# Kernel optimization log

Hardware: AMD Instinct MI355X
Metric: run time of the kernel (lower is better)

Reference implementation:

```python
import jax, jax.numpy as jnp
import numpy as np
from jax import lax

FC = 8      # heads_count
LN_EPS = 1e-5

def _ln(x, g, b):
    mu = jnp.mean(x, axis=-1, keepdims=True)
    var = jnp.mean((x - mu) ** 2, axis=-1, keepdims=True)
    return (x - mu) / jnp.sqrt(var + LN_EPS) * g + b

def _l2norm(x):
    return x / jnp.maximum(jnp.linalg.norm(x, axis=-1, keepdims=True), 1e-12)

def _gelu(x):
    return jax.nn.gelu(x, approximate=False)

def _resize_bilinear(x, oh, ow):
    # x: [N, C, H, W], align_corners=True bilinear (matches F.interpolate)
    h, w = x.shape[2], x.shape[3]
    ys = jnp.linspace(0.0, h - 1.0, oh)
    xs = jnp.linspace(0.0, w - 1.0, ow)
    y0 = jnp.floor(ys).astype(jnp.int32); y1 = jnp.minimum(y0 + 1, h - 1)
    x0 = jnp.floor(xs).astype(jnp.int32); x1 = jnp.minimum(x0 + 1, w - 1)
    dy = (ys - y0).astype(x.dtype)[None, None, :, None]
    dx = (xs - x0).astype(x.dtype)[None, None, None, :]
    rows = x[:, :, y0, :] * (1 - dy) + x[:, :, y1, :] * dy
    return rows[:, :, :, x0] * (1 - dx) + rows[:, :, :, x1] * dx

def _merge_block(x, center, h, w, p):
    # x: [n,l,c], center: [n,s,c]
    n, l, c = x.shape
    hc, wc = h // 2, w // 2
    xn = x.transpose(0, 2, 1).reshape(n, c, h, w)
    cn = center.transpose(0, 2, 1).reshape(n, c, hc, wc)
    up = _resize_bilinear(cn, h, w)
    y = jnp.concatenate([xn, up], axis=1)            # [n,2c,h,w]
    y = y.transpose(0, 2, 3, 1)                      # NHWC
    y = _gelu(y @ p['mb_l0_w'] + p['mb_l0_b'])
    y = y @ p['mb_l1_w'] + p['mb_l1_b']              # [n,h,w,c]
    y = y.transpose(0, 3, 1, 2)                      # NCHW
    mu = jnp.mean(y, axis=(1, 2, 3), keepdims=True)  # GroupNorm(1, c)
    var = jnp.mean((y - mu) ** 2, axis=(1, 2, 3), keepdims=True)
    y = (y - mu) / jnp.sqrt(var + LN_EPS) * p['mb_gn_g'][None, :, None, None] + p['mb_gn_b'][None, :, None, None]
    down = _resize_bilinear(y, hc, wc)
    new_x = y.reshape(n, c, h * w).transpose(0, 2, 1) + x
    new_c = down.reshape(n, c, hc * wc).transpose(0, 2, 1) + center
    return new_x, new_c

def _global_cluster(x0, center1, p):
    n, l, c = x0.shape
    s = center1.shape[1]
    xp = x0 @ p['gc_p0_w'] + p['gc_p0_b']            # [n,l,hd]
    cp = center1 @ p['gc_p1_w'] + p['gc_p1_b']       # [n,s,2hd]
    hd = xp.shape[-1]
    sc = hd // FC
    m = n * FC
    xp = xp.reshape(n, l, FC, sc).transpose(0, 2, 1, 3).reshape(m, l, sc)
    cp = cp.reshape(n, s, FC, 2 * sc).transpose(0, 2, 1, 3).reshape(m, s, 2 * sc)
    cpt, cval = cp[..., :sc], cp[..., sc:]
    sim = jnp.einsum('mlc,msc->mls', _l2norm(xp), _l2norm(cpt))
    sim = jax.nn.sigmoid(p['gc_alpha'] * sim + p['gc_beta'])
    vals = jnp.max(sim, axis=2)                      # [m,l]
    idx = jnp.argmax(sim, axis=2)                    # [m,l]
    disp = vals[..., None] * jnp.take_along_axis(cval, idx[:, :, None], axis=1)  # [m,l,sc]
    disp = disp.reshape(n, FC, l, sc).transpose(0, 2, 1, 3).reshape(n, l, FC * sc)
    return disp @ p['gc_m_w'] + p['gc_m_b']

def _global_block(x0, center1, h, w, p):
    n, l, c = x0.shape
    new = _global_cluster(x0, center1, p)
    new = _ln(new, p['gb_n0_g'], p['gb_n0_b'])
    y = jnp.concatenate([x0, new], axis=2)           # [n,l,2c]
    y = y.reshape(n, h, w, 2 * c)
    y = _gelu(y @ p['gb_lin_w'] + p['gb_lin_b'])     # [n,h,w,2c]
    y = y.transpose(0, 3, 1, 2)                      # NCHW
    y = lax.conv_general_dilated(y, p['gb_conv_w'], (1, 1), ((1, 1), (1, 1)),
                                 dimension_numbers=('NCHW', 'OIHW', 'NCHW'))
    y = y + p['gb_conv_b'][None, :, None, None]
    y = y.reshape(n, c, h * w).transpose(0, 2, 1)    # [n,l,c]
    return _ln(y, p['gb_n1_g'], p['gb_n1_b']) + x0

def setup_inputs() -> dict:
    key = jax.random.key(0)
    ks = jax.random.split(key, 24)
    N, H, W, C, HD = 8, 52, 52, 256, 256
    L = H * W
    S = (H // 2) * (W // 2)
    f32 = jnp.float32
    def xav(k, shape, fin, fout):
        a = (6.0 / (fin + fout)) ** 0.5
        return jax.random.uniform(k, shape, minval=-a, maxval=a, dtype=f32)
    return {
        'x0_16x': jax.random.normal(ks[0], (N, L, C), f32),
        'x1_16x': jax.random.normal(ks[1], (N, L, C), f32),
        'x0_32x': jax.random.normal(ks[2], (N, S, C), f32),
        'x1_32x': jax.random.normal(ks[3], (N, S, C), f32),
        'size0_16x': 52, 'size1_16x': 52,
        'mb_l0_w': xav(ks[4], (2 * C, 2 * C), 2 * C, 2 * C), 'mb_l0_b': jnp.zeros((2 * C,), f32),
        'mb_l1_w': xav(ks[5], (2 * C, C), 2 * C, C), 'mb_l1_b': jnp.zeros((C,), f32),
        'mb_gn_g': jnp.ones((C,), f32), 'mb_gn_b': jnp.zeros((C,), f32),
        'gc_p0_w': xav(ks[6], (C, HD), C, HD), 'gc_p0_b': jnp.zeros((HD,), f32),
        'gc_p1_w': xav(ks[7], (C, 2 * HD), C, 2 * HD), 'gc_p1_b': jnp.zeros((2 * HD,), f32),
        'gc_m_w': xav(ks[8], (HD, C), HD, C), 'gc_m_b': jnp.zeros((C,), f32),
        'gc_alpha': jnp.ones((1,), f32), 'gc_beta': jnp.zeros((1,), f32),
        'gb_n0_g': jnp.ones((C,), f32), 'gb_n0_b': jnp.zeros((C,), f32),
        'gb_lin_w': xav(ks[9], (2 * C, 2 * C), 2 * C, 2 * C), 'gb_lin_b': jnp.zeros((2 * C,), f32),
        'gb_conv_w': xav(ks[10], (C, 2 * C, 3, 3), 2 * C * 9, C * 9), 'gb_conv_b': jnp.zeros((C,), f32),
        'gb_n1_g': jnp.ones((C,), f32), 'gb_n1_b': jnp.zeros((C,), f32),
    }

def reference(x0_16x, x1_16x, x0_32x, x1_32x, size0_16x, size1_16x,
              mb_l0_w, mb_l0_b, mb_l1_w, mb_l1_b, mb_gn_g, mb_gn_b,
              gc_p0_w, gc_p0_b, gc_p1_w, gc_p1_b, gc_m_w, gc_m_b, gc_alpha, gc_beta,
              gb_n0_g, gb_n0_b, gb_lin_w, gb_lin_b, gb_conv_w, gb_conv_b, gb_n1_g, gb_n1_b):
    p = dict(mb_l0_w=mb_l0_w, mb_l0_b=mb_l0_b, mb_l1_w=mb_l1_w, mb_l1_b=mb_l1_b,
             mb_gn_g=mb_gn_g, mb_gn_b=mb_gn_b,
             gc_p0_w=gc_p0_w, gc_p0_b=gc_p0_b, gc_p1_w=gc_p1_w, gc_p1_b=gc_p1_b,
             gc_m_w=gc_m_w, gc_m_b=gc_m_b, gc_alpha=gc_alpha, gc_beta=gc_beta,
             gb_n0_g=gb_n0_g, gb_n0_b=gb_n0_b, gb_lin_w=gb_lin_w, gb_lin_b=gb_lin_b,
             gb_conv_w=gb_conv_w, gb_conv_b=gb_conv_b, gb_n1_g=gb_n1_g, gb_n1_b=gb_n1_b)
    h0 = w0 = int(size0_16x)
    h1 = w1 = int(size1_16x)
    # single layer, type == 'cross' (types=["cross"]); shared weights across streams
    x0_16x, x0_32x = _merge_block(x0_16x, x0_32x, h0, w0, p)
    x1_16x, x1_32x = _merge_block(x1_16x, x1_32x, h1, w1, p)
    x0_16x = _global_block(x0_16x, x1_32x, h0, w0, p)
    x1_16x = _global_block(x1_16x, x0_32x, h1, w1, p)
    return (x0_16x, x1_16x)
```

## Files before the change

kernel.cpp:

```cpp
#include <hip/hip_runtime.h>
#include <math.h>

#define NB 8
#define HH 52
#define WW 52
#define LL 2704
#define CC 256
#define HC 26
#define WC 26
#define SS 676
#define C2 512
#define FCn 8
#define SCn 32
#define M16 (NB*LL)
#define M32 (NB*SS)
#define KCONV (9*C2)
#define SAMP16 ((size_t)LL*CC)
#define SAMP32 ((size_t)SS*CC)

typedef double dvec4 __attribute__((ext_vector_type(4)));
typedef float  f32x4 __attribute__((ext_vector_type(4)));
typedef short  b16x8 __attribute__((ext_vector_type(8)));

__device__ __forceinline__ float  gelu_ct(float x){ return 0.5f*x*(1.0f + erff(x*0.70710678118654752f)); }
__device__ __forceinline__ double gelu_ct(double x){ return 0.5*x*(1.0 + erf(x*0.70710678118654752440)); }

__device__ __forceinline__ short f2b(float x){
    union { float f; unsigned u; } v; v.f = x;
    unsigned r = v.u + 0x7fffu + ((v.u >> 16) & 1u);
    return (short)(r >> 16);
}

template<typename TA0, typename TO, bool GELU, bool ADDB, bool UPS>
__global__ __launch_bounds__(256) void gemm_d64(
    const TA0* __restrict__ A0,
    const float* __restrict__ W, const float* __restrict__ Bias,
    const double* __restrict__ cw,
    TO* __restrict__ Out, int M, int K, int N)
{
    __shared__ double As[16][130];
    __shared__ double Bs[16][66];
    const int t = threadIdx.x;
    const int mBase = blockIdx.y * 128;
    const int nBase = blockIdx.x * 64;
    const int arow = t >> 1;
    const int kofA = (t & 1) << 3;
    const int kb   = t >> 4;
    const int nof  = (t & 15) << 2;
    const int w  = t >> 6;
    const int lane = t & 63;
    const int lr = lane & 15, lk = lane >> 4;

    dvec4 prm = {0.,0.,0.,0.}, prn = {0.,0.,0.,0.};
    prm = __builtin_amdgcn_mfma_f64_16x16x4f64((double)lr, 0.25, prm, 0,0,0);
    prn = __builtin_amdgcn_mfma_f64_16x16x4f64(0.25, (double)lr, prn, 0,0,0);
    int pm[4], pn[4];
    #pragma unroll
    for (int i=0;i<4;i++){ pm[i] = (int)prm[i]; pn[i] = (int)prn[i]; }

    dvec4 acc[2][4];
    #pragma unroll
    for (int rf=0;rf<2;rf++)
        #pragma unroll
        for (int cb=0;cb<4;cb++) acc[rf][cb] = (dvec4){0.,0.,0.,0.};

    const int am = mBase + arow;
    double aReg[8], bReg[4];
    auto loadA = [&](int k0){
        #pragma unroll
        for (int j=0;j<8;j++){
            int k = k0 + kofA + j;
            aReg[j] = (am < M) ? (double)A0[(size_t)am*K + k] : 0.0;
        }
    };
    auto loadB = [&](int k0){
        #pragma unroll
        for (int j=0;j<4;j++)
            bReg[j] = (double)W[(size_t)(k0+kb)*N + nBase + nof + j];
    };
    loadA(0); loadB(0);
    for (int k0 = 0; k0 < K; k0 += 16){
        __syncthreads();
        #pragma unroll
        for (int j=0;j<8;j++) As[kofA+j][arow] = aReg[j];
        #pragma unroll
        for (int j=0;j<4;j++) Bs[kb][nof+j] = bReg[j];
        __syncthreads();
        if (k0 + 16 < K){ loadA(k0+16); loadB(k0+16); }
        #pragma unroll
        for (int ks = 0; ks < 4; ks++){
            double a0 = As[ks*4+lk][w*32 + lr];
            double a1 = As[ks*4+lk][w*32 + 16 + lr];
            double b0 = Bs[ks*4+lk][lr];
            double b1 = Bs[ks*4+lk][16 + lr];
            double b2 = Bs[ks*4+lk][32 + lr];
            double b3 = Bs[ks*4+lk][48 + lr];
            acc[0][0] = __builtin_amdgcn_mfma_f64_16x16x4f64(a0,b0,acc[0][0],0,0,0);
            acc[0][1] = __builtin_amdgcn_mfma_f64_16x16x4f64(a0,b1,acc[0][1],0,0,0);
            acc[0][2] = __builtin_amdgcn_mfma_f64_16x16x4f64(a0,b2,acc[0][2],0,0,0);
            acc[0][3] = __builtin_amdgcn_mfma_f64_16x16x4f64(a0,b3,acc[0][3],0,0,0);
            acc[1][0] = __builtin_amdgcn_mfma_f64_16x16x4f64(a1,b0,acc[1][0],0,0,0);
            acc[1][1] = __builtin_amdgcn_mfma_f64_16x16x4f64(a1,b1,acc[1][1],0,0,0);
            acc[1][2] = __builtin_amdgcn_mfma_f64_16x16x4f64(a1,b2,acc[1][2],0,0,0);
            acc[1][3] = __builtin_amdgcn_mfma_f64_16x16x4f64(a1,b3,acc[1][3],0,0,0);
        }
    }
    #pragma unroll
    for (int rf=0;rf<2;rf++){
        #pragma unroll
        for (int i=0;i<4;i++){
            const int row = mBase + w*32 + rf*16 + pm[i];
            if (row >= M) continue;
            int nloc = 0, y0=0, y1=0, x0=0, x1=0;
            double dy=0.0, dx=0.0;
            if (UPS){
                nloc = row / LL;
                int l = row - nloc*LL;
                int hh = l / WW, ww2 = l - hh*WW;
                double fy = (hh==HH-1) ? (double)(HC-1) : hh*((double)(HC-1)/(HH-1));
                double fx = (ww2==WW-1) ? (double)(WC-1) : ww2*((double)(WC-1)/(WW-1));
                y0 = (int)fy; y1 = min(y0+1, HC-1);
                x0 = (int)fx; x1 = min(x0+1, WC-1);
                dy = fy - y0; dx = fx - x0;
            }
            #pragma unroll
            for (int cb=0;cb<4;cb++){
                const int col = nBase + cb*16 + pn[i];
                double v = acc[rf][cb][i];
                if (UPS){
                    const double* cb0 = cw + ((size_t)nloc*SS)*N + col;
                    double v00 = cb0[(size_t)(y0*WC + x0)*N];
                    double v01 = cb0[(size_t)(y0*WC + x1)*N];
                    double v10 = cb0[(size_t)(y1*WC + x0)*N];
                    double v11 = cb0[(size_t)(y1*WC + x1)*N];
                    double r0 = v00*(1.0-dy) + v10*dy;
                    double r1 = v01*(1.0-dy) + v11*dy;
                    v += r0*(1.0-dx) + r1*dx;
                }
                if (ADDB) v += (double)Bias[col];
                if (GELU) v = gelu_ct(v);
                Out[(size_t)row*N + col] = (TO)v;
            }
        }
    }
}

template<bool GELU, bool CAT, bool OUT_BF>
__global__ __launch_bounds__(256) void gemm_bf(
    const short* __restrict__ A0, const short* __restrict__ A1, int K0,
    const short* __restrict__ Wb, const float* __restrict__ Bias,
    void* __restrict__ OutV, int M, int K, int N)
{
    __shared__ short As[64][72];
    __shared__ short Bs[64][72];
    const int t = threadIdx.x;
    const int mBase = blockIdx.y*64, nBase = blockIdx.x*64;
    const int lane = t & 63, lr = lane & 15, lg = lane >> 4;
    const int wr = (t >> 6) * 16;
    const int srow = t >> 2;
    const int sk   = (t & 3) * 16;
    const int am = mBase + srow;
    const int bo = nBase + srow;
    f32x4 acc[4] = {{0,0,0,0},{0,0,0,0},{0,0,0,0},{0,0,0,0}};

    for (int c0 = 0; c0 < K; c0 += 64){
        const int kk = c0 + sk;
        const short* ap;
        if (!CAT || kk < K0) ap = A0 + (size_t)am*K0 + kk;
        else                 ap = A1 + (size_t)am*(K-K0) + (kk - K0);
        b16x8 a0 = *(const b16x8*)ap;
        b16x8 a1 = *(const b16x8*)(ap + 8);
        b16x8 bv0 = *(const b16x8*)&Wb[(size_t)bo*K + kk];
        b16x8 bv1 = *(const b16x8*)&Wb[(size_t)bo*K + kk + 8];
        __syncthreads();
        *(b16x8*)&As[srow][sk]     = a0;
        *(b16x8*)&As[srow][sk + 8] = a1;
        *(b16x8*)&Bs[srow][sk]     = bv0;
        *(b16x8*)&Bs[srow][sk + 8] = bv1;
        __syncthreads();
        #pragma unroll
        for (int kc=0;kc<2;kc++){
            b16x8 a = *(const b16x8*)&As[wr + lr][kc*32 + lg*8];
            #pragma unroll
            for (int cb=0;cb<4;cb++){
                b16x8 b = *(const b16x8*)&Bs[cb*16 + lr][kc*32 + lg*8];
                acc[cb] = __builtin_amdgcn_mfma_f32_16x16x32_bf16(a, b, acc[cb], 0,0,0);
            }
        }
    }
    #pragma unroll
    for (int cb=0;cb<4;cb++){
        int col = nBase + cb*16 + lr;
        float bias = Bias[col];
        #pragma unroll
        for (int i=0;i<4;i++){
            int row = mBase + wr + lg*4 + i;
            float v = acc[cb][i] + bias;
            if (GELU) v = gelu_ct(v);
            if (OUT_BF) ((short*)OutV)[(size_t)row*N + col] = f2b(v);
            else        ((float*)OutV)[(size_t)row*N + col] = v;
        }
    }
}

__global__ __launch_bounds__(256) void conv_bf2(const short* __restrict__ Xb,
    const short* __restrict__ WTb, const float* __restrict__ Bias, float* __restrict__ Out)
{
    __shared__ short As[32][72];
    __shared__ short Bs[256][72];
    const int t = threadIdx.x;
    const int mBase = blockIdx.x*32;
    const int lane = t & 63, lr = lane & 15, lg = lane >> 4;
    const int w = t >> 6;
    const int wr16 = (w & 1) * 16;
    const int ch   = (w >> 1) * 8;
    const int arow = t >> 3;
    const int ska  = (t & 7) * 8;
    const int srow = t >> 2;
    const int sk   = (t & 3) * 16;
    const int am = mBase + arow;
    const int an = am / LL; const int ahw = am % LL;
    const int ah = ahw / WW; const int aw = ahw % WW;
    f32x4 acc[8];
    #pragma unroll
    for (int i=0;i<8;i++) acc[i] = (f32x4){0.f,0.f,0.f,0.f};
    const b16x8 z = {0,0,0,0,0,0,0,0};

    for (int pos = 0; pos < 9; pos++){
        const int dh = pos/3 - 1, dw = pos%3 - 1;
        const int h2 = ah + dh, w2 = aw + dw;
        const bool ok = (h2 >= 0 && h2 < HH && w2 >= 0 && w2 < WW);
        const short* xrow = Xb + ((size_t)(an*LL + h2*WW + w2))*C2;
        for (int c0 = 0; c0 < C2; c0 += 64){
            b16x8 a0 = ok ? *(const b16x8*)&xrow[c0 + ska] : z;
            b16x8 w0[4], w1[4];
            #pragma unroll
            for (int r=0;r<4;r++){
                const short* wp = WTb + (size_t)(srow + 64*r)*KCONV + pos*C2 + c0 + sk;
                w0[r] = *(const b16x8*)wp;
                w1[r] = *(const b16x8*)(wp + 8);
            }
            __syncthreads();
            *(b16x8*)&As[arow][ska] = a0;
            #pragma unroll
            for (int r=0;r<4;r++){
                *(b16x8*)&Bs[srow + 64*r][sk]     = w0[r];
                *(b16x8*)&Bs[srow + 64*r][sk + 8] = w1[r];
            }
            __syncthreads();
            #pragma unroll
            for (int kc=0;kc<2;kc++){
                b16x8 a = *(const b16x8*)&As[wr16 + lr][kc*32 + lg*8];
                #pragma unroll
                for (int cb=0;cb<8;cb++){
                    b16x8 b = *(const b16x8*)&Bs[(ch+cb)*16 + lr][kc*32 + lg*8];
                    acc[cb] = __builtin_amdgcn_mfma_f32_16x16x32_bf16(a, b, acc[cb], 0,0,0);
                }
            }
        }
    }
    #pragma unroll
    for (int cb=0;cb<8;cb++){
        int col = (ch+cb)*16 + lr;
        float bias = Bias[col];
        #pragma unroll
        for (int i=0;i<4;i++){
            int row = mBase + wr16 + lg*4 + i;
            Out[(size_t)row*CC + col] = acc[cb][i] + bias;
        }
    }
}

__global__ void wtransb_k(const float* __restrict__ wsrc, short* __restrict__ wt){
    int o = blockIdx.x;
    int i = threadIdx.x;
    #pragma unroll
    for (int pos = 0; pos < 9; pos++)
        wt[(size_t)o*KCONV + pos*C2 + i] = f2b(wsrc[((size_t)o*C2 + i)*9 + pos]);
}

__global__ void wtb_k(const float* __restrict__ src, short* __restrict__ dst, int K, int N){
    int n = blockIdx.x;
    for (int k = threadIdx.x; k < K; k += 256)
        dst[(size_t)n*K + k] = f2b(src[(size_t)k*N + n]);
}

__global__ void d2b_k(const double* __restrict__ src, short* __restrict__ dst){
    int i = blockIdx.x*256 + threadIdx.x;
    dst[i] = f2b((float)src[i]);
}

__global__ __launch_bounds__(256) void gn_stats_k(const double* __restrict__ t2c,
    double* __restrict__ stats, int nOff){
    const double* p = t2c + (size_t)blockIdx.y*SAMP16;
    int i0 = blockIdx.x*4096 + threadIdx.x;
    double s = 0.0, q = 0.0;
    #pragma unroll
    for (int r = 0; r < 16; r++){
        double v = p[i0 + r*256];
        s += v; q += v*v;
    }
    #pragma unroll
    for (int off = 32; off; off >>= 1){
        s += __shfl_xor(s, off);
        q += __shfl_xor(q, off);
    }
    __shared__ double ls[4], lq[4];
    int wid = threadIdx.x >> 6;
    if ((threadIdx.x & 63) == 0){ ls[wid] = s; lq[wid] = q; }
    __syncthreads();
    if (threadIdx.x == 0){
        int n = nOff + blockIdx.y;
        atomicAdd(&stats[n*2+0], ls[0]+ls[1]+ls[2]+ls[3]);
        atomicAdd(&stats[n*2+1], lq[0]+lq[1]+lq[2]+lq[3]);
    }
}

__global__ void merge_x_k(const double* __restrict__ t2c, const float* __restrict__ x,
    const float* __restrict__ g, const float* __restrict__ b,
    const double* __restrict__ stats, int nOff, double* __restrict__ mxn){
    int idx = blockIdx.x*256 + threadIdx.x;
    const double inv = 1.0/((double)LL*CC);
    int c = idx & (CC-1);
    int n = nOff + idx / (LL*CC);
    double mu = stats[2*n]*inv;
    double var = stats[2*n+1]*inv - mu*mu;
    double r = 1.0/sqrt(var + 1e-5);
    mxn[idx] = (t2c[idx]-mu)*r*(double)g[c] + (double)b[c] + (double)x[idx];
}

__global__ void merge_c_k(const double* __restrict__ t2c, const float* __restrict__ cen,
    const float* __restrict__ g, const float* __restrict__ b,
    const double* __restrict__ stats, int nOff, double* __restrict__ mcn){
    int idx = blockIdx.x*256 + threadIdx.x;
    int c = idx & 255;
    int ns = idx >> 8;
    int nl = ns / SS, s = ns % SS;
    int i = s / WC, j = s % WC;
    double fy = (i==WC-1) ? (double)(HH-1) : i*((double)(HH-1)/(HC-1));
    double fx = (j==WC-1) ? (double)(WW-1) : j*((double)(WW-1)/(WC-1));
    int y0 = (int)fy; int y1 = min(y0+1, HH-1);
    int x0 = (int)fx; int x1 = min(x0+1, WW-1);
    double dy = fy - y0, dx = fx - x0;
    const double* base = t2c + (size_t)nl*SAMP16 + c;
    double v00 = base[(size_t)(y0*WW + x0)*CC];
    double v01 = base[(size_t)(y0*WW + x1)*CC];
    double v10 = base[(size_t)(y1*WW + x0)*CC];
    double v11 = base[(size_t)(y1*WW + x1)*CC];
    double r0 = v00*(1.0-dy) + v10*dy;
    double r1 = v01*(1.0-dy) + v11*dy;
    double v = r0*(1.0-dx) + r1*dx;
    const double inv = 1.0/((double)LL*CC);
    int n = nOff + nl;
    double mu = stats[2*n]*inv;
    double var = stats[2*n+1]*inv - mu*mu;
    double r = 1.0/sqrt(var + 1e-5);
    mcn[idx] = (v-mu)*r*(double)g[c] + (double)b[c] + (double)cen[idx];
}

__global__ __launch_bounds__(256) void cptn_k(const double* __restrict__ cp, double* __restrict__ ctn){
    int ns = blockIdx.x;
    int n = ns / SS, s = ns % SS;
    int hgrp = threadIdx.x >> 5, k = threadIdx.x & 31;
    double v = cp[(size_t)ns*C2 + hgrp*64 + k];
    double q = v*v;
    #pragma unroll
    for (int off = 16; off; off >>= 1) q += __shfl_xor(q, off, 32);
    double d = fmax(sqrt(q), 1e-12);
    ctn[((size_t)(n*FCn + hgrp)*SS + s)*SCn + k] = v/d;
}

__global__ __launch_bounds__(256) void norm_k(const double* __restrict__ xpc, double* __restrict__ norms){
    int t = threadIdx.x;
    int g = t >> 5, k = t & 31;
    int gl = blockIdx.x*8 + g;
    int nl = gl / LL, l = gl % LL;
    int h = blockIdx.y;
    double v = xpc[(size_t)gl*CC + h*SCn + k];
    double q = v*v;
    #pragma unroll
    for (int off = 16; off; off >>= 1) q += __shfl_xor(q, off, 32);
    if (k == 0) norms[((size_t)nl*FCn + h)*LL + l] = fmax(sqrt(q), 1e-12);
}

__global__ __launch_bounds__(256) void sim3_k(
    const double* __restrict__ xpc,
    const double* __restrict__ norms,
    const double* __restrict__ ctn,
    const double* __restrict__ cp,
    const float* __restrict__ alpha_p, const float* __restrict__ beta_p,
    int nOff, short* __restrict__ dispb)
{
    __shared__ double xs[32][65];
    __shared__ double cs[32][65];
    const int t = threadIdx.x;
    const int lBase = blockIdx.x * 64;
    const int h = blockIdx.y;
    const int nl = blockIdx.z;
    const int n = nOff + nl;
    const int w  = t >> 6;
    const int wr = (w >> 1) * 32;
    const int wc = (w & 1) * 32;
    const int lane = t & 63;
    const int lr = lane & 15, lk = lane >> 4;
    const double alpha = (double)alpha_p[0], beta = (double)beta_p[0];
    const double sgn = (alpha >= 0.0) ? 1.0 : -1.0;

    dvec4 prm = {0.,0.,0.,0.}, prn = {0.,0.,0.,0.};
    prm = __builtin_amdgcn_mfma_f64_16x16x4f64((double)lr, 0.25, prm, 0,0,0);
    prn = __builtin_amdgcn_mfma_f64_16x16x4f64(0.25, (double)lr, prn, 0,0,0);
    int pm[4], pn[4];
    #pragma unroll
    for (int i=0;i<4;i++){ pm[i] = (int)prm[i]; pn[i] = (int)prn[i]; }

    const int lav = min(64, LL - lBase);
    #pragma unroll
    for (int r = 0; r < 8; r++){
        int idx = t + r*256;
        int li = idx >> 5, ki = idx & 31;
        double v = 0.0;
        if (li < lav) v = xpc[((size_t)nl*LL + lBase + li)*CC + h*SCn + ki];
        xs[ki][li] = v;
    }

    double bz[2][2][4];
    int    bs[2][2][4];
    #pragma unroll
    for (int rf=0; rf<2; rf++)
        #pragma unroll
        for (int j=0; j<2; j++)
            #pragma unroll
            for (int i=0; i<4; i++){ bz[rf][j][i] = -1.0e300; bs[rf][j][i] = 0; }

    const double* cbase = ctn + ((size_t)(n*FCn + h))*SS*SCn;
    for (int sBase = 0; sBase < SS; sBase += 64){
        const int sav = min(64, SS - sBase);
        const double* cb = cbase + (size_t)sBase*SCn;
        __syncthreads();
        #pragma unroll
        for (int r = 0; r < 8; r++){
            int idx = t + r*256;
            int si = idx >> 5, ki = idx & 31;
            cs[ki][si] = (si < sav) ? cb[idx] : 0.0;
        }
        __syncthreads();
        dvec4 a00 = {0.,0.,0.,0.}, a01 = {0.,0.,0.,0.};
        dvec4 a10 = {0.,0.,0.,0.}, a11 = {0.,0.,0.,0.};
        #pragma unroll
        for (int ks = 0; ks < 8; ks++){
            double xa0 = xs[ks*4+lk][wr+lr];
            double xa1 = xs[ks*4+lk][wr+16+lr];
            double cb0 = cs[ks*4+lk][wc+lr];
            double cb1 = cs[ks*4+lk][wc+16+lr];
            a00 = __builtin_amdgcn_mfma_f64_16x16x4f64(xa0,cb0,a00,0,0,0);
            a01 = __builtin_amdgcn_mfma_f64_16x16x4f64(xa0,cb1,a01,0,0,0);
            a10 = __builtin_amdgcn_mfma_f64_16x16x4f64(xa1,cb0,a10,0,0,0);
            a11 = __builtin_amdgcn_mfma_f64_16x16x4f64(xa1,cb1,a11,0,0,0);
        }
        #pragma unroll
        for (int i=0;i<4;i++){
            int s0 = sBase + wc + pn[i];
            int s1 = s0 + 16;
            if (s0 < SS){
                double z = sgn*a00[i];
                if (z > bz[0][0][i]){ bz[0][0][i] = z; bs[0][0][i] = s0; }
                z = sgn*a10[i];
                if (z > bz[1][0][i]){ bz[1][0][i] = z; bs[1][0][i] = s0; }
            }
            if (s1 < SS){
                double z = sgn*a01[i];
                if (z > bz[0][1][i]){ bz[0][1][i] = z; bs[0][1][i] = s1; }
                z = sgn*a11[i];
                if (z > bz[1][1][i]){ bz[1][1][i] = z; bs[1][1][i] = s1; }
            }
        }
    }
    __syncthreads();
    double* redv = &xs[0][0];
    int*    redi = (int*)&cs[0][0];
    #pragma unroll
    for (int rf=0; rf<2; rf++){
        #pragma unroll
        for (int i=0;i<4;i++){
            double z0 = bz[rf][0][i]; int i0 = bs[rf][0][i];
            double z1 = bz[rf][1][i]; int i1 = bs[rf][1][i];
            bool take1 = (z1 > z0) || (z1 == z0 && i1 < i0);
            double z = take1 ? z1 : z0;
            int    s = take1 ? i1 : i0;
            int row = wr + rf*16 + pm[i];
            int cls = (w & 1)*16 + pn[i];
            redv[row*32 + cls] = z;
            redi[row*32 + cls] = s;
        }
    }
    __syncthreads();
    if (t < 64){
        double best = redv[t*32]; int bi = redi[t*32];
        #pragma unroll
        for (int c = 1; c < 32; c++){
            double v = redv[t*32 + c]; int ii = redi[t*32 + c];
            if (v > best || (v == best && ii < bi)){ best = v; bi = ii; }
        }
        int l = lBase + t;
        if (l < LL){
            double nrm = norms[((size_t)nl*FCn + h)*LL + l];
            double zb = alpha*((sgn*best)/nrm) + beta;
            double val;
            if (zb >= 0.0) val = 1.0/(1.0 + exp(-zb));
            else { double e = exp(zb); val = e/(1.0+e); }
            const double* cv = cp + ((size_t)(n*SS + bi))*C2 + h*64 + 32;
            short* dr = dispb + ((size_t)(n*LL + l))*CC + h*SCn;
            #pragma unroll
            for (int k=0;k<32;k++) dr[k] = f2b((float)(val*cv[k]));
        }
    }
}

__global__ __launch_bounds__(256) void ln_bf_k(const float* __restrict__ y,
    const float* __restrict__ g, const float* __restrict__ b, short* __restrict__ ob){
    int row = blockIdx.x*4 + (threadIdx.x >> 6);
    int lane = threadIdx.x & 63;
    const float* rp = y + (size_t)row*CC;
    float4 v = *(const float4*)(rp + lane*4);
    float s = v.x+v.y+v.z+v.w;
    float q = v.x*v.x+v.y*v.y+v.z*v.z+v.w*v.w;
    #pragma unroll
    for (int off = 32; off; off >>= 1){ s += __shfl_xor(s, off); q += __shfl_xor(q, off); }
    float mu = s*(1.0f/CC);
    float var = q*(1.0f/CC) - mu*mu;
    float r = rsqrtf(var + 1e-5f);
    int c = lane*4;
    float4 gv = *(const float4*)(g+c);
    float4 bv = *(const float4*)(b+c);
    short* op = ob + (size_t)row*CC + c;
    op[0] = f2b((v.x-mu)*r*gv.x+bv.x);
    op[1] = f2b((v.y-mu)*r*gv.y+bv.y);
    op[2] = f2b((v.z-mu)*r*gv.z+bv.z);
    op[3] = f2b((v.w-mu)*r*gv.w+bv.w);
}

__global__ __launch_bounds__(256) void final_k(float* __restrict__ y, const double* __restrict__ res,
    const float* __restrict__ g, const float* __restrict__ b){
    int row = blockIdx.x*4 + (threadIdx.x >> 6);
    int lane = threadIdx.x & 63;
    float* rp = y + (size_t)row*CC;
    const double* xp = res + (size_t)row*CC;
    float4 v = *(const float4*)(rp + lane*4);
    float s = v.x+v.y+v.z+v.w;
    float q = v.x*v.x+v.y*v.y+v.z*v.z+v.w*v.w;
    #pragma unroll
    for (int off = 32; off; off >>= 1){ s += __shfl_xor(s, off); q += __shfl_xor(q, off); }
    float mu = s*(1.0f/CC);
    float var = q*(1.0f/CC) - mu*mu;
    float r = rsqrtf(var + 1e-5f);
    int c = lane*4;
    float4 gv = *(const float4*)(g+c);
    float4 bv = *(const float4*)(b+c);
    float4 o;
    o.x = (v.x-mu)*r*gv.x+bv.x + (float)xp[c+0];
    o.y = (v.y-mu)*r*gv.y+bv.y + (float)xp[c+1];
    o.z = (v.z-mu)*r*gv.z+bv.z + (float)xp[c+2];
    o.w = (v.w-mu)*r*gv.w+bv.w + (float)xp[c+3];
    *(float4*)(rp+c) = o;
}

extern "C" void kernel_launch(void* const* d_in, const int* in_sizes, int n_in,
                              void* d_out, int out_size, void* d_ws, size_t ws_size,
                              hipStream_t stream)
{
    const float* x16[2] = {(const float*)d_in[0], (const float*)d_in[1]};
    const float* x32[2] = {(const float*)d_in[2], (const float*)d_in[3]};
    const float* mb_l0_w = (const float*)d_in[6];
    const float* mb_l0_b = (const float*)d_in[7];
    const float* mb_l1_w = (const float*)d_in[8];
    const float* mb_l1_b = (const float*)d_in[9];
    const float* mb_gn_g = (const float*)d_in[10];
    const float* mb_gn_b = (const float*)d_in[11];
    const float* gc_p0_w = (const float*)d_in[12];
    const float* gc_p0_b = (const float*)d_in[13];
    const float* gc_p1_w = (const float*)d_in[14];
    const float* gc_p1_b = (const float*)d_in[15];
    const float* gc_m_w  = (const float*)d_in[16];
    const float* gc_m_b  = (const float*)d_in[17];
    const float* gc_alpha= (const float*)d_in[18];
    const float* gc_beta = (const float*)d_in[19];
    const float* gb_n0_g = (const float*)d_in[20];
    const float* gb_n0_b = (const float*)d_in[21];
    const float* gb_lin_w= (const float*)d_in[22];
    const float* gb_lin_b= (const float*)d_in[23];
    const float* gb_conv_w=(const float*)d_in[24];
    const float* gb_conv_b=(const float*)d_in[25];
    const float* gb_n1_g = (const float*)d_in[26];
    const float* gb_n1_b = (const float*)d_in[27];

    const size_t F8  = (size_t)M16*CC*8;
    const size_t G8  = (size_t)M32*CC*8;
    const size_t WT4 = (size_t)KCONV*CC*4;

    char* base = (char*)d_ws;
    double* mx[2] = { (double*)base, (double*)(base + F8) };
    double* mc[2] = { (double*)(base + 2*F8), (double*)(base + 2*F8 + G8) };
    char*   pWT   = base + 2*F8 + 2*G8;
    short*  WTb   = (short*)pWT;
    short*  WLb   = (short*)(pWT + 2359296);
    short*  WMb   = (short*)(pWT + 2883584);
    double* stats = (double*)(pWT + WT4);
    char*   E     = pWT + WT4 + 256;
    const size_t base_need = 2*F8 + 2*G8 + WT4 + 256;

    const size_t T2  = (size_t)LL*CC*8;
    const size_t T1  = (size_t)LL*C2*8;
    const size_t TC  = (size_t)SS*C2*8;
    const size_t TN  = (size_t)FCn*LL*8;
    int nb = 1;
    {
        const int cands[4] = {8,4,2,1};
        for (int ci = 0; ci < 4; ci++){
            int c = cands[ci];
            size_t merge_r  = (size_t)c*(T2 + T1 + TC);
            size_t global_r = 22151168ull + 11075584ull + (size_t)c*(T2 + TN) + 11075584ull + 11075584ull;
            size_t r = merge_r > global_r ? merge_r : global_r;
            if (base_need + r <= ws_size){ nb = c; break; }
            if (c == 1) return;
        }
    }

    double* t2c = (double*)E;
    double* t1c = (double*)(E + nb*T2);
    double* cwb = (double*)(E + nb*(T2 + T1));
    double* cp    = (double*)E;
    double* ctn   = (double*)(E + 22151168);
    double* xpc   = (double*)(E + 33226752);
    double* norms = (double*)(E + 33226752 + nb*T2);
    short*  dispb = (short*) (E + 33226752 + (size_t)nb*(T2 + TN));
    short*  mxb   = (short*) (E + 33226752 + (size_t)nb*(T2 + TN) + 11075584);
    float*  Dbuf  = (float*) E;
    short*  Dbufb = (short*) (E + 22151168);
    short*  Bbufb = (short*) E;

    wtransb_k<<<CC, C2, 0, stream>>>(gb_conv_w, WTb);
    wtb_k<<<C2, 256, 0, stream>>>(gb_lin_w, WLb, C2, C2);
    wtb_k<<<CC, 256, 0, stream>>>(gc_m_w, WMb, CC, CC);

    const int Mc = nb*LL;
    const int Ms = nb*SS;
    const int mTiles  = (Mc + 127) / 128;
    const int sTiles  = (Ms + 127) / 128;

    for (int i = 0; i < 2; i++){
        hipMemsetAsync(stats, 0, 16*sizeof(double), stream);
        for (int ch = 0; ch < NB; ch += nb){
            const float* x16c = x16[i] + (size_t)ch*SAMP16;
            const float* x32c = x32[i] + (size_t)ch*SAMP32;
            gemm_d64<float,double,false,false,false><<<dim3(8, sTiles), 256, 0, stream>>>(
                x32c, mb_l0_w + (size_t)CC*C2, mb_l0_b, nullptr, cwb, Ms, CC, C2);
            gemm_d64<float,double,true,true,true><<<dim3(8, mTiles), 256, 0, stream>>>(
                x16c, mb_l0_w, mb_l0_b, cwb, t1c, Mc, CC, C2);
            gemm_d64<double,double,false,true,false><<<dim3(4, mTiles), 256, 0, stream>>>(
                t1c, mb_l1_w, mb_l1_b, nullptr, t2c, Mc, C2, CC);
            gn_stats_k<<<dim3(169, nb), 256, 0, stream>>>(t2c, stats, ch);
            merge_x_k<<<nb*LL, 256, 0, stream>>>(t2c, x16c,
                mb_gn_g, mb_gn_b, stats, ch, mx[i] + (size_t)ch*SAMP16);
            merge_c_k<<<nb*SS, 256, 0, stream>>>(t2c, x32c,
                mb_gn_g, mb_gn_b, stats, ch, mc[i] + (size_t)ch*SAMP32);
        }
    }

    float* outp[2] = { (float*)d_out, (float*)d_out + (size_t)M16*CC };
    for (int i = 0; i < 2; i++){
        const double* xi64 = mx[i];
        const double* ci64 = mc[1-i];
        gemm_d64<double,double,false,true,false><<<dim3(8, (M32+127)/128), 256, 0, stream>>>(
            ci64, gc_p1_w, gc_p1_b, nullptr, cp, M32, CC, C2);
        cptn_k<<<M32, 256, 0, stream>>>(cp, ctn);
        for (int ch = 0; ch < NB; ch += nb){
            gemm_d64<double,double,false,true,false><<<dim3(4, mTiles), 256, 0, stream>>>(
                xi64 + (size_t)ch*SAMP16, gc_p0_w, gc_p0_b, nullptr, xpc, Mc, CC, CC);
            norm_k<<<dim3(nb*(LL/8), FCn), 256, 0, stream>>>(xpc, norms);
            sim3_k<<<dim3((LL+63)/64, FCn, nb), 256, 0, stream>>>(
                xpc, norms, ctn, cp, gc_alpha, gc_beta, ch, dispb);
        }
        d2b_k<<<(M16*CC)/256, 256, 0, stream>>>(xi64, mxb);
        gemm_bf<false,false,false><<<dim3(4, 338), 256, 0, stream>>>(
            dispb, (const short*)nullptr, CC, WMb, gc_m_b, Dbuf, M16, CC, CC);
        ln_bf_k<<<M16/4, 256, 0, stream>>>(Dbuf, gb_n0_g, gb_n0_b, Dbufb);
        gemm_bf<true,true,true><<<dim3(8, 338), 256, 0, stream>>>(
            mxb, Dbufb, CC, WLb, gb_lin_b, Bbufb, M16, C2, C2);
        conv_bf2<<<M16/32, 256, 0, stream>>>(Bbufb, WTb, gb_conv_b, outp[i]);
        final_k<<<M16/4, 256, 0, stream>>>(outp[i], xi64, gb_n1_g, gb_n1_b);
    }
}
```

Baseline: 2.490 ms.

## Fuse row-norm into similarity kernel and batch gc_p0 projection across streams

Drops the separate norm_k kernel and its norms buffer. The per-row L2 norm is now computed inside sim3_k from the tile already staged in shared memory, at the cost of one extra barrier and a small reduction. When workspace allows, the gc_p0 projection for both streams runs as one larger GEMM before the loop, and sim3_k runs over all samples in a single launch. This removes launch overhead and gives larger grids, but needs a bigger xpc buffer; otherwise the old chunked path is used.

```diff
diff --git a/kernel.cpp b/kernel.cpp
--- a/kernel.cpp
+++ b/kernel.cpp
@@ -370,22 +370,8 @@
     ctn[((size_t)(n*FCn + hgrp)*SS + s)*SCn + k] = v/d;
 }
 
-__global__ __launch_bounds__(256) void norm_k(const double* __restrict__ xpc, double* __restrict__ norms){
-    int t = threadIdx.x;
-    int g = t >> 5, k = t & 31;
-    int gl = blockIdx.x*8 + g;
-    int nl = gl / LL, l = gl % LL;
-    int h = blockIdx.y;
-    double v = xpc[(size_t)gl*CC + h*SCn + k];
-    double q = v*v;
-    #pragma unroll
-    for (int off = 16; off; off >>= 1) q += __shfl_xor(q, off, 32);
-    if (k == 0) norms[((size_t)nl*FCn + h)*LL + l] = fmax(sqrt(q), 1e-12);
-}
-
 __global__ __launch_bounds__(256) void sim3_k(
     const double* __restrict__ xpc,
-    const double* __restrict__ norms,
     const double* __restrict__ ctn,
     const double* __restrict__ cp,
     const float* __restrict__ alpha_p, const float* __restrict__ beta_p,
@@ -393,6 +379,7 @@
 {
     __shared__ double xs[32][65];
     __shared__ double cs[32][65];
+    __shared__ double redn[4][64];
     const int t = threadIdx.x;
     const int lBase = blockIdx.x * 64;
     const int h = blockIdx.y;
@@ -422,6 +409,20 @@
         if (li < lav) v = xpc[((size_t)nl*LL + lBase + li)*CC + h*SCn + ki];
         xs[ki][li] = v;
     }
+    __syncthreads();
+    {
+        int li = t & 63, q4 = t >> 6;
+        double part = 0.0;
+        #pragma unroll
+        for (int ki = 0; ki < 8; ki++){
+            double v = xs[q4*8 + ki][li];
+            part += v*v;
+        }
+        redn[q4][li] = part;
+    }
+    __syncthreads();
+    double myNrm = 1e-12;
+    if (t < 64) myNrm = fmax(sqrt(redn[0][t]+redn[1][t]+redn[2][t]+redn[3][t]), 1e-12);
 
     double bz[2][2][4];
     int    bs[2][2][4];
@@ -503,8 +504,7 @@
         }
         int l = lBase + t;
         if (l < LL){
-            double nrm = norms[((size_t)nl*FCn + h)*LL + l];
-            double zb = alpha*((sgn*best)/nrm) + beta;
+            double zb = alpha*((sgn*best)/myNrm) + beta;
             double val;
             if (zb >= 0.0) val = 1.0/(1.0 + exp(-zb));
             else { double e = exp(zb); val = e/(1.0+e); }
@@ -611,19 +611,20 @@
     const size_t T2  = (size_t)LL*CC*8;
     const size_t T1  = (size_t)LL*C2*8;
     const size_t TC  = (size_t)SS*C2*8;
-    const size_t TN  = (size_t)FCn*LL*8;
     int nb = 1;
     {
         const int cands[4] = {8,4,2,1};
         for (int ci = 0; ci < 4; ci++){
             int c = cands[ci];
             size_t merge_r  = (size_t)c*(T2 + T1 + TC);
-            size_t global_r = 22151168ull + 11075584ull + (size_t)c*(T2 + TN) + 11075584ull + 11075584ull;
+            size_t global_r = 55377920ull + (size_t)c*T2;
             size_t r = merge_r > global_r ? merge_r : global_r;
             if (base_need + r <= ws_size){ nb = c; break; }
             if (c == 1) return;
         }
     }
+    const size_t XPC2 = 2ull*NB*T2;
+    const bool combined = (base_need + 55377920ull + XPC2 <= ws_size);
 
     double* t2c = (double*)E;
     double* t1c = (double*)(E + nb*T2);
@@ -631,9 +632,9 @@
     double* cp    = (double*)E;
     double* ctn   = (double*)(E + 22151168);
     double* xpc   = (double*)(E + 33226752);
-    double* norms = (double*)(E + 33226752 + nb*T2);
-    short*  dispb = (short*) (E + 33226752 + (size_t)nb*(T2 + TN));
-    short*  mxb   = (short*) (E + 33226752 + (size_t)nb*(T2 + TN) + 11075584);
+    const size_t xsz = combined ? XPC2 : (size_t)nb*T2;
+    short*  dispb = (short*) (E + 33226752 + xsz);
+    short*  mxb   = (short*) (E + 33226752 + xsz + 11075584);
     float*  Dbuf  = (float*) E;
     short*  Dbufb = (short*) (E + 22151168);
     short*  Bbufb = (short*) E;
@@ -667,18 +668,26 @@
     }
 
     float* outp[2] = { (float*)d_out, (float*)d_out + (size_t)M16*CC };
+    if (combined){
+        gemm_d64<double,double,false,true,false><<<dim3(4, (2*M16+127)/128), 256, 0, stream>>>(
+            mx[0], gc_p0_w, gc_p0_b, nullptr, xpc, 2*M16, CC, CC);
+    }
     for (int i = 0; i < 2; i++){
         const double* xi64 = mx[i];
         const double* ci64 = mc[1-i];
         gemm_d64<double,double,false,true,false><<<dim3(8, (M32+127)/128), 256, 0, stream>>>(
             ci64, gc_p1_w, gc_p1_b, nullptr, cp, M32, CC, C2);
         cptn_k<<<M32, 256, 0, stream>>>(cp, ctn);
-        for (int ch = 0; ch < NB; ch += nb){
-            gemm_d64<double,double,false,true,false><<<dim3(4, mTiles), 256, 0, stream>>>(
-                xi64 + (size_t)ch*SAMP16, gc_p0_w, gc_p0_b, nullptr, xpc, Mc, CC, CC);
-            norm_k<<<dim3(nb*(LL/8), FCn), 256, 0, stream>>>(xpc, norms);
-            sim3_k<<<dim3((LL+63)/64, FCn, nb), 256, 0, stream>>>(
-                xpc, norms, ctn, cp, gc_alpha, gc_beta, ch, dispb);
+        if (combined){
+            sim3_k<<<dim3((LL+63)/64, FCn, NB), 256, 0, stream>>>(
+                xpc + (size_t)i*NB*SAMP16, ctn, cp, gc_alpha, gc_beta, 0, dispb);
+        } else {
+            for (int ch = 0; ch < NB; ch += nb){
+                gemm_d64<double,double,false,true,false><<<dim3(4, mTiles), 256, 0, stream>>>(
+                    xi64 + (size_t)ch*SAMP16, gc_p0_w, gc_p0_b, nullptr, xpc, Mc, CC, CC);
+                sim3_k<<<dim3((LL+63)/64, FCn, nb), 256, 0, stream>>>(
+                    xpc, ctn, cp, gc_alpha, gc_beta, ch, dispb);
+            }
         }
         d2b_k<<<(M16*CC)/256, 256, 0, stream>>>(xi64, mxb);
         gemm_bf<false,false,false><<<dim3(4, 338), 256, 0, stream>>>(
```

Measured after the change: 2.518 ms. Within noise of the previous version (+1.1%).
